# Kernel tuning notes

Measured on AMD Instinct MI355X. Metric: run time of the kernel, lower is better.

Reference implementation:

```python
import jax, jax.numpy as jnp
import numpy as np
import math

PHI = (1.0 + math.sqrt(5.0)) / 2.0
KAPPA = 0.5
B_, L_, D_, N_, R_ = 4, 1024, 768, 16, 48  # batch, seq, d_model, state_size, dt_rank


@jax.custom_vjp
def fractal_pow(mag, exponent):
    # |h|^e with torch _FractalCompress semantics (clamped-ratio grad, no grad wrt e)
    return jnp.maximum(mag, 1e-8) ** exponent


def _fp_fwd(mag, exponent):
    mag_safe = jnp.maximum(mag, 1e-8)
    compressed = mag_safe ** exponent
    ratio = exponent * compressed / (mag_safe + 1e-10)
    return compressed, ratio


def _fp_bwd(ratio, g):
    return (g * jnp.minimum(ratio, 5.0), jnp.zeros_like(ratio))


fractal_pow.defvjp(_fp_fwd, _fp_bwd)


def setup_inputs() -> dict:
    key = jax.random.key(0)
    ks = jax.random.split(key, 7)

    def u(k, shape, fan_in):
        b = (1.0 / PHI) / math.sqrt(fan_in)
        return jax.random.uniform(k, shape, jnp.float32, -b, b)

    x = jax.random.normal(ks[0], (B_, L_, D_), dtype=jnp.float32)
    in_proj_w = u(ks[1], (D_, 2 * D_), D_)          # Linear(D, 2D, bias=False), stored (in,out)
    x_proj_w = u(ks[2], (D_, R_ + 4 * N_), D_)      # Linear(D, dt_rank + 2*N*2, bias=False)
    dt_proj_w = u(ks[3], (R_, D_), R_)              # Linear(dt_rank, D)
    bb = 1.0 / math.sqrt(R_)
    dt_proj_b = jax.random.uniform(ks[4], (D_,), jnp.float32, -bb, bb)
    out_proj_w = u(ks[5], (D_, D_), D_)             # Linear(D, D)
    ob = 1.0 / math.sqrt(D_)
    out_proj_b = jax.random.uniform(ks[6], (D_,), jnp.float32, -ob, ob)
    # phi-scaled A init (exact torch init)
    n_slow = round(N_ / PHI)
    n_fast = N_ - n_slow
    A_init = np.concatenate([np.linspace(0.5, 2.0, n_slow), np.linspace(2.0, float(N_), n_fast)])
    A_log = jnp.asarray(np.log(A_init), dtype=jnp.float32)
    return dict(x=x, in_proj_w=in_proj_w, x_proj_w=x_proj_w, dt_proj_w=dt_proj_w,
                dt_proj_b=dt_proj_b, out_proj_w=out_proj_w, out_proj_b=out_proj_b, A_log=A_log)


def _forward(x, in_proj_w, x_proj_w, dt_proj_w, dt_proj_b, out_proj_w, out_proj_b, A_log):
    B, L, D = x.shape
    N = A_log.shape[0]
    R = dt_proj_w.shape[0]

    xz = x @ in_proj_w                               # (B,L,2D)
    x_in = jax.nn.silu(xz[..., :D])
    z = xz[..., D:]
    xp = x_in @ x_proj_w                             # (B,L,R+4N)
    dt = jax.nn.softplus(xp[..., :R] @ dt_proj_w + dt_proj_b)  # (B,L,D)
    bc = xp[..., R:].reshape(B, L, 2, N, 2)
    Bm, Cm = bc[:, :, 0], bc[:, :, 1]                # (B,L,N,2) each

    # dna_init: 16 phases, magnitude 0.01
    phases = jnp.linspace(0.0, 2.0 * math.pi * (1.0 - 1.0 / N), N)
    h0 = 0.01 * jnp.stack([jnp.cos(phases), jnp.sin(phases)], axis=-1)  # (N,2)
    h0 = jnp.broadcast_to(h0, (B, D, N, 2)) + jnp.zeros((B, D, N, 2), jnp.float32)
    A_neg = -jnp.exp(A_log)                          # (N,)

    def step(h, inp):
        x_t, dt_t, Bt, Ct = inp                      # (B,D),(B,D),(B,N,2),(B,N,2)
        alpha = jnp.exp(dt_t[..., None] * A_neg)     # (B,D,N)
        e = 1.0 + (1.0 - alpha) * KAPPA
        # fractal compress: |h|^e, phase preserved
        mag = jnp.sqrt(h[..., 0] ** 2 + h[..., 1] ** 2 + 1e-8)
        ph = jnp.arctan2(h[..., 1], h[..., 0] + 1e-10)
        cm = fractal_pow(mag, e)
        h = jnp.stack([cm * jnp.cos(ph), cm * jnp.sin(ph)], axis=-1)
        # h += gamma * B * x  (x is real, so complex mul is a scale of B)
        h = h + Bt[:, None, :, :] * (x_t * dt_t)[:, :, None, None]
        # tanh magnitude squash, phase preserved
        m2 = jnp.sqrt(h[..., 0] ** 2 + h[..., 1] ** 2 + 1e-8)
        p2 = jnp.arctan2(h[..., 1], h[..., 0] + 1e-10)
        s = jnp.tanh(m2)
        h = jnp.stack([s * jnp.cos(p2), s * jnp.sin(p2)], axis=-1)
        # y = Re(conj(C) * h).sum(N) = C_re*h_re + C_im*h_im summed over N
        y = jnp.sum(Ct[:, None, :, 0] * h[..., 0] + Ct[:, None, :, 1] * h[..., 1], axis=-1)
        return h, y

    xs = (x_in.swapaxes(0, 1), dt.swapaxes(0, 1), Bm.swapaxes(0, 1), Cm.swapaxes(0, 1))
    _, ys = jax.lax.scan(step, h0, xs)               # ys: (L,B,D)
    y = ys.swapaxes(0, 1) * jax.nn.silu(z)
    return y @ out_proj_w + out_proj_b


def reference(x, in_proj_w, x_proj_w, dt_proj_w, dt_proj_b, out_proj_w, out_proj_b, A_log):
    return _forward(x, in_proj_w, x_proj_w, dt_proj_w, dt_proj_b, out_proj_w, out_proj_b, A_log)
```

## Files before the change

### kernel.cpp

```cpp
#include <hip/hip_runtime.h>
#include <math.h>

#if __has_builtin(__builtin_amdgcn_exp2f)
#define EXP2F(x) __builtin_amdgcn_exp2f(x)
#else
#define EXP2F(x) exp2f(x)
#endif
#if __has_builtin(__builtin_amdgcn_logf)
#define LOG2F(x) __builtin_amdgcn_logf(x)
#else
#define LOG2F(x) log2f(x)
#endif
#if __has_builtin(__builtin_amdgcn_rcpf)
#define RCPF(x) __builtin_amdgcn_rcpf(x)
#else
#define RCPF(x) (1.0f / (x))
#endif

#define LOG2E 1.4426950408889634f

#define DRAIN_VMEM() asm volatile("s_waitcnt vmcnt(0)" ::: "memory")

typedef __bf16 bf16x8 __attribute__((ext_vector_type(8)));
typedef float f32x4 __attribute__((ext_vector_type(4)));

__device__ __forceinline__ float silu_f(float v) {
    return v * RCPF(1.0f + EXP2F(-v * LOG2E));
}
__device__ __forceinline__ float softplus_f(float v) {
    return fmaxf(v, 0.0f) + log1pf(__expf(-fabsf(v)));
}

template <int CTRL>
__device__ __forceinline__ float dpp_add(float v) {
    int r = __builtin_amdgcn_update_dpp(0, __float_as_int(v), CTRL, 0xF, 0xF, true);
    return v + __int_as_float(r);
}

__device__ __forceinline__ unsigned short bf16_rne(float f) {
    unsigned int u = __float_as_uint(f);
    return (unsigned short)((u + 0x7FFFu + ((u >> 16) & 1u)) >> 16);
}
__device__ __forceinline__ unsigned short bf16_hi(float f, float& rem) {
    unsigned int u = __float_as_uint(f);
    unsigned int hb = (u + 0x7FFFu + ((u >> 16) & 1u)) >> 16;
    rem = f - __uint_as_float(hb << 16);
    return (unsigned short)hb;
}

__device__ __forceinline__ void async_g2l16(const void* g, void* l) {
    __builtin_amdgcn_global_load_lds(
        (const __attribute__((address_space(1))) unsigned int*)g,
        (__attribute__((address_space(3))) unsigned int*)l, 16, 0, 0);
}

__global__ __launch_bounds__(256) void conv_all_k(
    const float* __restrict__ x,
    unsigned short* __restrict__ xh,
    const float* __restrict__ w_in,
    unsigned short* __restrict__ wih, unsigned short* __restrict__ wil,
    const float* __restrict__ w_out,
    unsigned short* __restrict__ woh, unsigned short* __restrict__ wol,
    const float* __restrict__ w_xp,
    const float* __restrict__ w_dt,
    const float* __restrict__ b_dt,
    unsigned short* __restrict__ wbh, unsigned short* __restrict__ wbl,
    float* __restrict__ bias_full)
{
    __shared__ float shmem[6272];
    const int bid = blockIdx.x;
    const int t = threadIdx.x;
    if (bid < 768) {
#pragma unroll
        for (int r = 0; r < 4; ++r) {
            int i = (bid + 768 * r) * 256 + t;
            float4 v = ((const float4*)x)[i];
            ushort4 h;
            h.x = bf16_rne(v.x);
            h.y = bf16_rne(v.y);
            h.z = bf16_rne(v.z);
            h.w = bf16_rne(v.w);
            ((ushort4*)xh)[i] = h;
        }
        return;
    }
    if (bid < 2496) {
        const float* W;
        unsigned short *Th, *Tl;
        int N, bx, by;
        if (bid < 1920) {
            int b2 = bid - 768;
            W = w_in; Th = wih; Tl = wil; N = 1536;
            bx = b2 % 48; by = b2 / 48;
        } else {
            int b3 = bid - 1920;
            W = w_out; Th = woh; Tl = wol; N = 768;
            bx = b3 % 24; by = b3 / 24;
        }
        const int K = 768;
        float (*tile)[33] = (float (*)[33])shmem;
        const int tx = t & 31, ty = t >> 5;
        const int n0 = bx * 32, k0 = by * 32;
#pragma unroll
        for (int r = 0; r < 4; ++r)
            tile[ty + r * 8][tx] = W[(size_t)(k0 + ty + r * 8) * N + n0 + tx];
        __syncthreads();
#pragma unroll
        for (int r = 0; r < 4; ++r) {
            float v = tile[tx][ty + r * 8];
            float rem;
            unsigned short h = bf16_hi(v, rem);
            size_t o = (size_t)(n0 + ty + r * 8) * K + k0 + tx;
            Th[o] = h;
            Tl[o] = bf16_rne(rem);
        }
        return;
    }
    if (bid < 2640) {
        int b4 = bid - 2496;
        int bxw = b4 % 12, byw = b4 / 12;
        const int kd0 = byw * 64, dd0 = bxw * 64;
        float* As = shmem;
        float* Ws = shmem + 64 * 49;
        {
            int r = t >> 2;
            int c4 = (t & 3) * 4;
#pragma unroll
            for (int s = 0; s < 3; ++s) {
                float4 a = *(const float4*)&w_xp[(size_t)(kd0 + r) * 112 + c4 + 16 * s];
                As[r * 49 + c4 + 16 * s + 0] = a.x;
                As[r * 49 + c4 + 16 * s + 1] = a.y;
                As[r * 49 + c4 + 16 * s + 2] = a.z;
                As[r * 49 + c4 + 16 * s + 3] = a.w;
            }
            int rw = t >> 4;
            int cw = (t & 15) * 4;
#pragma unroll
            for (int s = 0; s < 3; ++s) {
                float4 w = *(const float4*)&w_dt[(size_t)(rw + 16 * s) * 768 + dd0 + cw];
                Ws[(rw + 16 * s) * 65 + cw + 0] = w.x;
                Ws[(rw + 16 * s) * 65 + cw + 1] = w.y;
                Ws[(rw + 16 * s) * 65 + cw + 2] = w.z;
                Ws[(rw + 16 * s) * 65 + cw + 3] = w.w;
            }
        }
        __syncthreads();
        const int ty = t >> 4, tx = t & 15;
        float acc[4][4];
#pragma unroll
        for (int i = 0; i < 4; ++i)
#pragma unroll
            for (int j = 0; j < 4; ++j) acc[i][j] = 0.0f;
        for (int k = 0; k < 48; ++k) {
            float ar[4], wr[4];
#pragma unroll
            for (int i = 0; i < 4; ++i) ar[i] = As[(ty * 4 + i) * 49 + k];
#pragma unroll
            for (int j = 0; j < 4; ++j) wr[j] = Ws[k * 65 + tx * 4 + j];
#pragma unroll
            for (int i = 0; i < 4; ++i)
#pragma unroll
                for (int j = 0; j < 4; ++j)
                    acc[i][j] = fmaf(ar[i], wr[j], acc[i][j]);
        }
        __syncthreads();
        float* Ot = shmem;
#pragma unroll
        for (int i = 0; i < 4; ++i)
#pragma unroll
            for (int j = 0; j < 4; ++j)
                Ot[(tx * 4 + j) * 65 + ty * 4 + i] = acc[i][j];
        __syncthreads();
        int dl = t >> 2, c0 = (t & 3) * 16;
#pragma unroll
        for (int k = 0; k < 16; ++k) {
            float v = Ot[dl * 65 + c0 + k];
            float rem;
            unsigned short h = bf16_hi(v, rem);
            size_t o = (size_t)(64 + dd0 + dl) * 768 + kd0 + c0 + k;
            wbh[o] = h;
            wbl[o] = bf16_rne(rem);
        }
        return;
    }
    if (bid < 2688) {
        int b5 = bid - 2640;
        int bxb = b5 & 1, byb = b5 >> 1;
        const int n0 = bxb * 32, k0 = byb * 32;
        float (*tile)[33] = (float (*)[33])shmem;
        const int tx = t & 31, ty = t >> 5;
#pragma unroll
        for (int r = 0; r < 4; ++r)
            tile[ty + r * 8][tx] = w_xp[(size_t)(k0 + ty + r * 8) * 112 + 48 + n0 + tx];
        __syncthreads();
#pragma unroll
        for (int r = 0; r < 4; ++r) {
            float v = tile[tx][ty + r * 8];
            float rem;
            unsigned short h = bf16_hi(v, rem);
            size_t o = (size_t)(n0 + ty + r * 8) * 768 + k0 + tx;
            wbh[o] = h;
            wbl[o] = bf16_rne(rem);
        }
        return;
    }
#pragma unroll
    for (int i = 0; i < 4; ++i) {
        int idx = t + 256 * i;
        if (idx < 896)
            bias_full[idx] = (idx >= 64 && idx < 832) ? b_dt[idx - 64] : 0.0f;
    }
}

template <int EPI, int WRX>
__global__ __launch_bounds__(256, 3) void mgemm_k(
    const unsigned short* __restrict__ Ah,
    const unsigned short* __restrict__ Bth, const unsigned short* __restrict__ Btl,
    const float* __restrict__ bias,
    float* __restrict__ C, int K, int ldc, int nby,
    unsigned short* __restrict__ xh, unsigned short* __restrict__ xl)
{
    __shared__ unsigned short smem[2][8192];

    const int t = threadIdx.x;
    const int wave = t >> 6, lane = t & 63;
    const int bx = blockIdx.x / nby, by = blockIdx.x % nby;
    const int bm = by * 128, bn = bx * 64;
    const int mw = (wave >> 1) * 64, nw = (wave & 1) * 32;

    const unsigned short* smat;
    int row0, lmoff;
    if      (wave == 0) { smat = Ah;  row0 = bm;      lmoff = 0; }
    else if (wave == 1) { smat = Ah;  row0 = bm + 64; lmoff = 2048 * 2; }
    else if (wave == 2) { smat = Bth; row0 = bn;      lmoff = 4096 * 2; }
    else                { smat = Btl; row0 = bn;      lmoff = 6144 * 2; }
    const int lr = lane >> 2;
    const int kq = (lane & 3) ^ ((lane >> 3) & 3);
    const unsigned short* gbase = smat + (size_t)(row0 + lr) * K + kq * 8;

    const int la = lane & 15, g4 = lane >> 4;
    const int fo = (g4 ^ ((la >> 1) & 3)) * 8;
    const int aoff = (mw + la) * 32 + fo;
    const int boff = (nw + la) * 32 + fo;

    f32x4 acc[4][2];
#pragma unroll
    for (int i = 0; i < 4; ++i)
#pragma unroll
        for (int j = 0; j < 2; ++j) acc[i][j] = (f32x4){0.f, 0.f, 0.f, 0.f};

    auto stage = [&](int buf, int k0) {
        char* lm = (char*)&smem[buf][0] + lmoff;
        const unsigned short* g = gbase + k0;
#pragma unroll
        for (int j = 0; j < 4; ++j)
            async_g2l16(g + (size_t)j * 16 * K, lm + j * 1024);
    };

    stage(0, 0);
    DRAIN_VMEM();
    __syncthreads();

    for (int k0 = 0; k0 < K; k0 += 32) {
        const int cur = (k0 >> 5) & 1;
        if (k0 + 32 < K) stage(cur ^ 1, k0 + 32);

        const unsigned short* base = &smem[cur][0];
        const unsigned short* pAh = base + aoff;
        const unsigned short* pBh = base + 4096 + boff;
        const unsigned short* pBl = base + 6144 + boff;

        bf16x8 fah[4], fbh[2], fbl[2];
#pragma unroll
        for (int i = 0; i < 4; ++i)
            fah[i] = *(const bf16x8*)(pAh + i * 512);
#pragma unroll
        for (int j = 0; j < 2; ++j) {
            fbh[j] = *(const bf16x8*)(pBh + j * 512);
            fbl[j] = *(const bf16x8*)(pBl + j * 512);
        }
#pragma unroll
        for (int i = 0; i < 4; ++i)
#pragma unroll
            for (int j = 0; j < 2; ++j)
                acc[i][j] = __builtin_amdgcn_mfma_f32_16x16x32_bf16(fah[i], fbh[j], acc[i][j], 0, 0, 0);
#pragma unroll
        for (int i = 0; i < 4; ++i)
#pragma unroll
            for (int j = 0; j < 2; ++j)
                acc[i][j] = __builtin_amdgcn_mfma_f32_16x16x32_bf16(fah[i], fbl[j], acc[i][j], 0, 0, 0);
        DRAIN_VMEM();
        __syncthreads();
    }

#pragma unroll
    for (int i = 0; i < 4; ++i) {
        int row = bm + mw + i * 16 + g4 * 4;
#pragma unroll
        for (int j = 0; j < 2; ++j) {
            int col = bn + nw + j * 16 + la;
            float bz = bias ? bias[col] : 0.0f;
#pragma unroll
            for (int r = 0; r < 4; ++r) {
                float v = acc[i][j][r] + bz;
                if (EPI == 1) v = silu_f(v);
                C[(size_t)(row + r) * ldc + col] = v;
                if (WRX) {
                    if (col < 768) {
                        float rem;
                        unsigned short hh = bf16_hi(v, rem);
                        xh[(size_t)(row + r) * 768 + col] = hh;
                        xl[(size_t)(row + r) * 768 + col] = bf16_rne(rem);
                    }
                }
            }
        }
    }
}

__global__ __launch_bounds__(256, 3) void mgemm3_k(
    const unsigned short* __restrict__ Ahp, const unsigned short* __restrict__ Alp,
    const unsigned short* __restrict__ Bth, const unsigned short* __restrict__ Btl,
    const float* __restrict__ bias,
    float* __restrict__ C, int K, int ldc, int nby)
{
    __shared__ unsigned short smem[2][12288];

    const int t = threadIdx.x;
    const int wave = t >> 6, lane = t & 63;
    const int bx = blockIdx.x / nby, by = blockIdx.x % nby;
    const int bm = by * 128, bn = bx * 64;
    const int mw = (wave >> 1) * 64, nw = (wave & 1) * 32;

    const unsigned short* smat;
    int row0, ninst, lmoff;
    if      (wave == 0) { smat = Ahp; row0 = bm; ninst = 8; lmoff = 0; }
    else if (wave == 1) { smat = Alp; row0 = bm; ninst = 8; lmoff = 8192; }
    else if (wave == 2) { smat = Bth; row0 = bn; ninst = 4; lmoff = 16384; }
    else                { smat = Btl; row0 = bn; ninst = 4; lmoff = 20480; }
    const int lr = lane >> 2;
    const int kq = (lane & 3) ^ ((lane >> 3) & 3);
    const unsigned short* gbase = smat + (size_t)(row0 + lr) * K + kq * 8;

    const int la = lane & 15, g4 = lane >> 4;
    const int fo = (g4 ^ ((la >> 1) & 3)) * 8;
    const int aoff = (mw + la) * 32 + fo;
    const int boff = (nw + la) * 32 + fo;

    f32x4 acc[4][2];
#pragma unroll
    for (int i = 0; i < 4; ++i)
#pragma unroll
        for (int j = 0; j < 2; ++j) acc[i][j] = (f32x4){0.f, 0.f, 0.f, 0.f};

    auto stage = [&](int buf, int k0) {
        char* lm = (char*)&smem[buf][0] + lmoff;
        const unsigned short* g = gbase + k0;
        if (ninst == 8) {
#pragma unroll
            for (int j = 0; j < 8; ++j)
                async_g2l16(g + (size_t)j * 16 * K, lm + j * 1024);
        } else {
#pragma unroll
            for (int j = 0; j < 4; ++j)
                async_g2l16(g + (size_t)j * 16 * K, lm + j * 1024);
        }
    };

    stage(0, 0);
    DRAIN_VMEM();
    __syncthreads();

    for (int k0 = 0; k0 < K; k0 += 32) {
        const int cur = (k0 >> 5) & 1;
        if (k0 + 32 < K) stage(cur ^ 1, k0 + 32);

        const unsigned short* base = &smem[cur][0];
        const unsigned short* pAh = base + aoff;
        const unsigned short* pAl = base + 4096 + aoff;
        const unsigned short* pBh = base + 8192 + boff;
        const unsigned short* pBl = base + 10240 + boff;

        bf16x8 fah[4], fal[4], fbh[2], fbl[2];
#pragma unroll
        for (int i = 0; i < 4; ++i) {
            fah[i] = *(const bf16x8*)(pAh + i * 512);
            fal[i] = *(const bf16x8*)(pAl + i * 512);
        }
#pragma unroll
        for (int j = 0; j < 2; ++j) {
            fbh[j] = *(const bf16x8*)(pBh + j * 512);
            fbl[j] = *(const bf16x8*)(pBl + j * 512);
        }
#pragma unroll
        for (int i = 0; i < 4; ++i)
#pragma unroll
            for (int j = 0; j < 2; ++j)
                acc[i][j] = __builtin_amdgcn_mfma_f32_16x16x32_bf16(fah[i], fbh[j], acc[i][j], 0, 0, 0);
#pragma unroll
        for (int i = 0; i < 4; ++i)
#pragma unroll
            for (int j = 0; j < 2; ++j)
                acc[i][j] = __builtin_amdgcn_mfma_f32_16x16x32_bf16(fah[i], fbl[j], acc[i][j], 0, 0, 0);
#pragma unroll
        for (int i = 0; i < 4; ++i)
#pragma unroll
            for (int j = 0; j < 2; ++j)
                acc[i][j] = __builtin_amdgcn_mfma_f32_16x16x32_bf16(fal[i], fbh[j], acc[i][j], 0, 0, 0);
        DRAIN_VMEM();
        __syncthreads();
    }

#pragma unroll
    for (int i = 0; i < 4; ++i) {
        int row = bm + mw + i * 16 + g4 * 4;
#pragma unroll
        for (int j = 0; j < 2; ++j) {
            int col = bn + nw + j * 16 + la;
            float bz = bias[col];
#pragma unroll
            for (int r = 0; r < 4; ++r) {
                float v = acc[i][j][r] + bz;
                if (col >= 64) v = softplus_f(v);
                C[(size_t)(row + r) * ldc + col] = v;
            }
        }
    }
}

#define L_LEN 1024
#define CH 32
#define NCH (L_LEN / CH)
#define CHP (CH + 4)

__global__ __launch_bounds__(512) void scan_k(
    const float* __restrict__ xz,
    const float* __restrict__ bcdt,
    const float* __restrict__ A_log,
    unsigned short* __restrict__ ybh)
{
    __shared__ float xdt_t[2][16][CHP];
    __shared__ float ds_t[2][16][CHP];
    __shared__ float B0s[2][16][CHP];
    __shared__ float B1s[2][16][CHP];
    __shared__ float C0s[2][16][CHP];
    __shared__ float C1s[2][16][CHP];
    __shared__ float ysp[2][CH][16][8];

    const int t  = threadIdx.x;
    const int b  = blockIdx.y;
    const int d0 = blockIdx.x * 16;
    const size_t rowbase = (size_t)b * L_LEN;
    const bool is_chain = (t < 256);

    const int n  = t & 15;
    const int dl = (t >> 4) & 15;
    const int np = n >> 1;
    float negAl2e = 0.0f, h0 = 0.0f, h1 = 0.0f;
    float s2 = 1.0f, lT = 0.0f;
    if (is_chain) {
        negAl2e = -__expf(A_log[n]) * LOG2E;
        float phase = 6.283185307179586f * (float)n / 16.0f;
        h0 = 0.01f * cosf(phase);
        h1 = 0.01f * sinf(phase);
        lT = LOG2F(fmaf(h0, h0, fmaf(h1, h1, 1e-8f)));
    }

    const int t2 = t - 256;
    const int hl = t2 >> 2;
    const int hf = (t2 & 3) * 4;

    auto stage = [&](int cc) {
        const int bi = cc & 1;
        if (t2 < 128) {
            size_t row = rowbase + cc * CH + hl;
            float4 rx = *(const float4*)&xz[row * 1536 + d0 + hf];
            float4 rd = *(const float4*)&bcdt[row * 896 + 64 + d0 + hf];
            xdt_t[bi][hf + 0][hl] = rx.x * rd.x;
            xdt_t[bi][hf + 1][hl] = rx.y * rd.y;
            xdt_t[bi][hf + 2][hl] = rx.z * rd.z;
            xdt_t[bi][hf + 3][hl] = rx.w * rd.w;
            ds_t[bi][hf + 0][hl] = rd.x;
            ds_t[bi][hf + 1][hl] = rd.y;
            ds_t[bi][hf + 2][hl] = rd.z;
            ds_t[bi][hf + 3][hl] = rd.w;
        }
#pragma unroll
        for (int i = 0; i < 2; ++i) {
            int idx = t2 + 256 * i;
            int lb = idx >> 4, j4 = (idx & 15) * 4;
            float4 rbc = *(const float4*)&bcdt[(rowbase + cc * CH + lb) * 896 + j4];
            if (j4 < 32) {
                int nn = j4 >> 1;
                B0s[bi][nn][lb]     = rbc.x;
                B1s[bi][nn][lb]     = rbc.y;
                B0s[bi][nn + 1][lb] = rbc.z;
                B1s[bi][nn + 1][lb] = rbc.w;
            } else {
                int nn = (j4 - 32) >> 1;
                C0s[bi][nn][lb]     = rbc.x;
                C1s[bi][nn][lb]     = rbc.y;
                C0s[bi][nn + 1][lb] = rbc.z;
                C1s[bi][nn + 1][lb] = rbc.w;
            }
        }
    };

    auto store_y = [&](int cs) {
        if (t2 >= 128) return;
        const int bi = cs & 1;
        size_t row = rowbase + cs * CH + hl;
        float4 zq = *(const float4*)&xz[row * 1536 + 768 + d0 + hf];
        float yr[4];
#pragma unroll
        for (int j = 0; j < 4; ++j) {
            float4 p0 = *(const float4*)&ysp[bi][hl][hf + j][0];
            float4 p1 = *(const float4*)&ysp[bi][hl][hf + j][4];
            yr[j] = ((p0.x + p0.y) + (p0.z + p0.w)) + ((p1.x + p1.y) + (p1.z + p1.w));
        }
        ushort4 hh;
        hh.x = bf16_rne(yr[0] * zq.x);
        hh.y = bf16_rne(yr[1] * zq.y);
        hh.z = bf16_rne(yr[2] * zq.z);
        hh.w = bf16_rne(yr[3] * zq.w);
        *(ushort4*)&ybh[row * 768 + d0 + hf] = hh;
    };

    if (!is_chain) stage(0);
    __syncthreads();

    for (int c = 0; c < NCH; ++c) {
        if (is_chain) {
            __builtin_amdgcn_s_setprio(1);
            const int bi = c & 1;
            const float* xr  = &xdt_t[bi][dl][0];
            const float* dr  = &ds_t[bi][dl][0];
            const float* b0r = &B0s[bi][n][0];
            const float* b1r = &B1s[bi][n][0];
            const float* c0r = &C0s[bi][n][0];
            const float* c1r = &C1s[bi][n][0];

            float4 px  = *(const float4*)(xr);
            float4 pd  = *(const float4*)(dr);
            float4 pb0 = *(const float4*)(b0r);
            float4 pb1 = *(const float4*)(b1r);
            float4 pc0 = *(const float4*)(c0r);
            float4 pc1 = *(const float4*)(c1r);

            for (int l4 = 0; l4 < CH; l4 += 4) {
                float4 cx = px, cd = pd, cb0 = pb0, cb1 = pb1, cc0 = pc0, cc1 = pc1;
                if (l4 + 4 < CH) {
                    px  = *(const float4*)(xr  + l4 + 4);
                    pd  = *(const float4*)(dr  + l4 + 4);
                    pb0 = *(const float4*)(b0r + l4 + 4);
                    pb1 = *(const float4*)(b1r + l4 + 4);
                    pc0 = *(const float4*)(c0r + l4 + 4);
                    pc1 = *(const float4*)(c1r + l4 + 4);
                }
                const float xv[4]  = {cx.x,  cx.y,  cx.z,  cx.w};
                const float dv[4]  = {cd.x,  cd.y,  cd.z,  cd.w};
                const float C0v[4] = {cc0.x, cc0.y, cc0.z, cc0.w};
                const float C1v[4] = {cc1.x, cc1.y, cc1.z, cc1.w};

                float cfv[4], bx0[4], bx1[4];
                const float B0v[4] = {cb0.x, cb0.y, cb0.z, cb0.w};
                const float B1v[4] = {cb1.x, cb1.y, cb1.z, cb1.w};
#pragma unroll
                for (int u = 0; u < 4; ++u) {
                    cfv[u] = fmaf(EXP2F(dv[u] * negAl2e), -0.25f, 0.25f);
                    bx0[u] = B0v[u] * xv[u];
                    bx1[u] = B1v[u] * xv[u];
                }

#pragma unroll
                for (int u = 0; u < 4; ++u) {
                    float g = s2 * EXP2F(cfv[u] * lT);
                    h0 = fmaf(h0, g, bx0[u]);
                    h1 = fmaf(h1, g, bx1[u]);
                    float q  = fmaf(h0, h0, fmaf(h1, h1, 1e-8f));
                    float q2 = q * q;
                    float num = fmaf(q2, q + 378.0f,              fmaf(17325.0f, q, 135135.0f));
                    float den = fmaf(q2, fmaf(28.0f, q, 3150.0f), fmaf(62370.0f, q, 135135.0f));
                    s2 = num * RCPF(den);
                    lT = LOG2F(s2 * s2 * q);

                    float yv = s2 * fmaf(C0v[u], h0, C1v[u] * h1);
                    yv = dpp_add<0xB1>(yv);
                    if ((n & 1) == 0) ysp[bi][l4 + u][dl][np] = yv;
                }
            }
            __builtin_amdgcn_s_setprio(0);
        } else {
            if (c + 1 < NCH) stage(c + 1);
            if (c >= 1) store_y(c - 1);
        }
        __syncthreads();
    }
    if (!is_chain) store_y(NCH - 1);
}

extern "C" void kernel_launch(void* const* d_in, const int* in_sizes, int n_in,
                              void* d_out, int out_size, void* d_ws, size_t ws_size,
                              hipStream_t stream)
{
    const float* x     = (const float*)d_in[0];
    const float* w_in  = (const float*)d_in[1];
    const float* w_xp  = (const float*)d_in[2];
    const float* w_dt  = (const float*)d_in[3];
    const float* b_dt  = (const float*)d_in[4];
    const float* w_out = (const float*)d_in[5];
    const float* b_out = (const float*)d_in[6];
    const float* A_log = (const float*)d_in[7];
    float* out = (float*)d_out;

    const int M = 4096;
    float* xz        = (float*)d_ws;
    float* bcdt      = xz + (size_t)M * 1536;
    float* bias_full = bcdt + (size_t)M * 896;
    unsigned short* ah   = (unsigned short*)(bias_full + 896);
    unsigned short* ybh  = ah   + (size_t)M * 768;
    unsigned short* xinh = ybh  + (size_t)M * 768;
    unsigned short* xinl = xinh + (size_t)M * 768;
    unsigned short* wh   = xinl + (size_t)M * 768;
    unsigned short* wl   = wh   + (size_t)1536 * 768;
    unsigned short* voh  = wl   + (size_t)1536 * 768;
    unsigned short* vol  = voh  + (size_t)768 * 768;
    unsigned short* wbh  = vol  + (size_t)768 * 768;
    unsigned short* wbl  = wbh  + (size_t)896 * 768;

    dim3 blk(256);

    conv_all_k<<<dim3(2689), blk, 0, stream>>>(
        x, ah, w_in, wh, wl, w_out, voh, vol,
        w_xp, w_dt, b_dt, wbh, wbl, bias_full);

    mgemm_k<1, 1><<<dim3(24 * 32), blk, 0, stream>>>(
        ah, wh, wl, (const float*)nullptr, xz, 768, 1536, 32, xinh, xinl);

    mgemm3_k<<<dim3(14 * 32), blk, 0, stream>>>(
        xinh, xinl, wbh, wbl, bias_full, bcdt, 768, 896, 32);

    scan_k<<<dim3(48, 4), dim3(512), 0, stream>>>(xz, bcdt, A_log, ybh);

    mgemm_k<0, 0><<<dim3(12 * 32), blk, 0, stream>>>(
        ybh, voh, vol, b_out, out, 768, 768, 32,
        (unsigned short*)nullptr, (unsigned short*)nullptr);
}
```

Baseline: 255.9 us.

## Triple-buffer LDS staging in split-bf16 GEMMs with partial vmcnt waits

Both MFMA GEMM kernels go from double to triple buffering of shared memory. Loads are issued two k-steps ahead, and each iteration waits only for the older batch of async loads (vmcnt(4) or vmcnt(8)) instead of draining every load. One barrier per iteration now sits before staging, which replaces the end-of-loop drain. This hides more global-load latency behind the MFMA work, at the cost of more LDS per block, and the launch-bounds occupancy hint for mgemm3_k drops from 3 to 2.

```diff
diff --git a/kernel.cpp b/kernel.cpp
--- a/kernel.cpp
+++ b/kernel.cpp
@@ -19,7 +19,9 @@
 
 #define LOG2E 1.4426950408889634f
 
-#define DRAIN_VMEM() asm volatile("s_waitcnt vmcnt(0)" ::: "memory")
+#define WAITVM0() asm volatile("s_waitcnt vmcnt(0)" ::: "memory")
+#define WAITVM4() asm volatile("s_waitcnt vmcnt(4)" ::: "memory")
+#define WAITVM8() asm volatile("s_waitcnt vmcnt(8)" ::: "memory")
 
 typedef __bf16 bf16x8 __attribute__((ext_vector_type(8)));
 typedef float f32x4 __attribute__((ext_vector_type(4)));
@@ -220,7 +222,7 @@
     float* __restrict__ C, int K, int ldc, int nby,
     unsigned short* __restrict__ xh, unsigned short* __restrict__ xl)
 {
-    __shared__ unsigned short smem[2][8192];
+    __shared__ unsigned short smem[3][8192];
 
     const int t = threadIdx.x;
     const int wave = t >> 6, lane = t & 63;
@@ -231,9 +233,9 @@
     const unsigned short* smat;
     int row0, lmoff;
     if      (wave == 0) { smat = Ah;  row0 = bm;      lmoff = 0; }
-    else if (wave == 1) { smat = Ah;  row0 = bm + 64; lmoff = 2048 * 2; }
-    else if (wave == 2) { smat = Bth; row0 = bn;      lmoff = 4096 * 2; }
-    else                { smat = Btl; row0 = bn;      lmoff = 6144 * 2; }
+    else if (wave == 1) { smat = Ah;  row0 = bm + 64; lmoff = 4096; }
+    else if (wave == 2) { smat = Bth; row0 = bn;      lmoff = 8192; }
+    else                { smat = Btl; row0 = bn;      lmoff = 12288; }
     const int lr = lane >> 2;
     const int kq = (lane & 3) ^ ((lane >> 3) & 3);
     const unsigned short* gbase = smat + (size_t)(row0 + lr) * K + kq * 8;
@@ -258,12 +260,16 @@
     };
 
     stage(0, 0);
-    DRAIN_VMEM();
-    __syncthreads();
-
+    if (32 < K) stage(1, 32);
+
+    int cur = 0, stg = 2;
     for (int k0 = 0; k0 < K; k0 += 32) {
-        const int cur = (k0 >> 5) & 1;
-        if (k0 + 32 < K) stage(cur ^ 1, k0 + 32);
+        if (k0 + 32 < K) { WAITVM4(); } else { WAITVM0(); }
+        __syncthreads();
+        if (k0 + 64 < K) {
+            stage(stg, k0 + 64);
+            stg = (stg == 2) ? 0 : stg + 1;
+        }
 
         const unsigned short* base = &smem[cur][0];
         const unsigned short* pAh = base + aoff;
@@ -289,8 +295,7 @@
 #pragma unroll
             for (int j = 0; j < 2; ++j)
                 acc[i][j] = __builtin_amdgcn_mfma_f32_16x16x32_bf16(fah[i], fbl[j], acc[i][j], 0, 0, 0);
-        DRAIN_VMEM();
-        __syncthreads();
+        cur = (cur == 2) ? 0 : cur + 1;
     }
 
 #pragma unroll
@@ -318,13 +323,13 @@
     }
 }
 
-__global__ __launch_bounds__(256, 3) void mgemm3_k(
+__global__ __launch_bounds__(256, 2) void mgemm3_k(
     const unsigned short* __restrict__ Ahp, const unsigned short* __restrict__ Alp,
     const unsigned short* __restrict__ Bth, const unsigned short* __restrict__ Btl,
     const float* __restrict__ bias,
     float* __restrict__ C, int K, int ldc, int nby)
 {
-    __shared__ unsigned short smem[2][12288];
+    __shared__ unsigned short smem[3][12288];
 
     const int t = threadIdx.x;
     const int wave = t >> 6, lane = t & 63;
@@ -368,12 +373,20 @@
     };
 
     stage(0, 0);
-    DRAIN_VMEM();
-    __syncthreads();
-
+    if (32 < K) stage(1, 32);
+
+    int cur = 0, stg = 2;
     for (int k0 = 0; k0 < K; k0 += 32) {
-        const int cur = (k0 >> 5) & 1;
-        if (k0 + 32 < K) stage(cur ^ 1, k0 + 32);
+        if (k0 + 32 < K) {
+            if (ninst == 8) { WAITVM8(); } else { WAITVM4(); }
+        } else {
+            WAITVM0();
+        }
+        __syncthreads();
+        if (k0 + 64 < K) {
+            stage(stg, k0 + 64);
+            stg = (stg == 2) ? 0 : stg + 1;
+        }
 
         const unsigned short* base = &smem[cur][0];
         const unsigned short* pAh = base + aoff;
@@ -407,8 +420,7 @@
 #pragma unroll
             for (int j = 0; j < 2; ++j)
                 acc[i][j] = __builtin_amdgcn_mfma_f32_16x16x32_bf16(fal[i], fbh[j], acc[i][j], 0, 0, 0);
-        DRAIN_VMEM();
-        __syncthreads();
+        cur = (cur == 2) ? 0 : cur + 1;
     }
 
 #pragma unroll
```

New measurement: 257.2 us. No clear change (+0.5%).

## Split weight conversion, fuse side conversions into in-proj GEMM, narrow GEMM tiles

Applied to the files above, without the earlier changes.

The combined conversion kernel is split. Only the x and in_proj conversions stay in front; the out_proj, x_proj/dt_proj and bias preparation move into extra blocks appended to the in_proj GEMM launch, so they run alongside it. The x_proj GEMM and the out_proj GEMM drop to 32-wide N tiles, which doubles their block counts so more CUs are busy. The trade-off is less reuse of each A tile per block and a less uniform mixed-work launch.

```diff
diff --git a/kernel.cpp b/kernel.cpp
--- a/kernel.cpp
+++ b/kernel.cpp
@@ -54,20 +54,13 @@
         (__attribute__((address_space(3))) unsigned int*)l, 16, 0, 0);
 }
 
-__global__ __launch_bounds__(256) void conv_all_k(
+__global__ __launch_bounds__(256) void conv_front_k(
     const float* __restrict__ x,
     unsigned short* __restrict__ xh,
     const float* __restrict__ w_in,
-    unsigned short* __restrict__ wih, unsigned short* __restrict__ wil,
-    const float* __restrict__ w_out,
-    unsigned short* __restrict__ woh, unsigned short* __restrict__ wol,
-    const float* __restrict__ w_xp,
-    const float* __restrict__ w_dt,
-    const float* __restrict__ b_dt,
-    unsigned short* __restrict__ wbh, unsigned short* __restrict__ wbl,
-    float* __restrict__ bias_full)
+    unsigned short* __restrict__ wih, unsigned short* __restrict__ wil)
 {
-    __shared__ float shmem[6272];
+    __shared__ float shmem[32 * 33];
     const int bid = blockIdx.x;
     const int t = threadIdx.x;
     if (bid < 768) {
@@ -84,40 +77,164 @@
         }
         return;
     }
-    if (bid < 2496) {
-        const float* W;
-        unsigned short *Th, *Tl;
-        int N, bx, by;
-        if (bid < 1920) {
-            int b2 = bid - 768;
-            W = w_in; Th = wih; Tl = wil; N = 1536;
-            bx = b2 % 48; by = b2 / 48;
-        } else {
-            int b3 = bid - 1920;
-            W = w_out; Th = woh; Tl = wol; N = 768;
-            bx = b3 % 24; by = b3 / 24;
-        }
-        const int K = 768;
+    int b2 = bid - 768;
+    const int N = 1536, K = 768;
+    float (*tile)[33] = (float (*)[33])shmem;
+    const int tx = t & 31, ty = t >> 5;
+    const int bx = b2 % 48, by = b2 / 48;
+    const int n0 = bx * 32, k0 = by * 32;
+#pragma unroll
+    for (int r = 0; r < 4; ++r)
+        tile[ty + r * 8][tx] = w_in[(size_t)(k0 + ty + r * 8) * N + n0 + tx];
+    __syncthreads();
+#pragma unroll
+    for (int r = 0; r < 4; ++r) {
+        float v = tile[tx][ty + r * 8];
+        float rem;
+        unsigned short h = bf16_hi(v, rem);
+        size_t o = (size_t)(n0 + ty + r * 8) * K + k0 + tx;
+        wih[o] = h;
+        wil[o] = bf16_rne(rem);
+    }
+}
+
+__global__ __launch_bounds__(256, 3) void gemm2t_k(
+    const unsigned short* __restrict__ Ah,
+    const unsigned short* __restrict__ Bth, const unsigned short* __restrict__ Btl,
+    float* __restrict__ C,
+    unsigned short* __restrict__ xh, unsigned short* __restrict__ xl,
+    const float* __restrict__ w_out,
+    unsigned short* __restrict__ woh, unsigned short* __restrict__ wol,
+    const float* __restrict__ w_xp,
+    const float* __restrict__ w_dt,
+    const float* __restrict__ b_dt,
+    unsigned short* __restrict__ wbh, unsigned short* __restrict__ wbl,
+    float* __restrict__ bias_full)
+{
+    __shared__ unsigned short smem[2][8192];
+
+    const int t = threadIdx.x;
+    const int bid = blockIdx.x;
+    const int K = 768, ldc = 1536, nby = 32;
+
+    if (bid < 768) {
+        const int wave = t >> 6, lane = t & 63;
+        const int bx = bid / nby, by = bid % nby;
+        const int bm = by * 128, bn = bx * 64;
+        const int mw = (wave >> 1) * 64, nw = (wave & 1) * 32;
+
+        const unsigned short* smat;
+        int row0, lmoff;
+        if      (wave == 0) { smat = Ah;  row0 = bm;      lmoff = 0; }
+        else if (wave == 1) { smat = Ah;  row0 = bm + 64; lmoff = 4096; }
+        else if (wave == 2) { smat = Bth; row0 = bn;      lmoff = 8192; }
+        else                { smat = Btl; row0 = bn;      lmoff = 12288; }
+        const int lr = lane >> 2;
+        const int kq = (lane & 3) ^ ((lane >> 3) & 3);
+        const unsigned short* gbase = smat + (size_t)(row0 + lr) * K + kq * 8;
+
+        const int la = lane & 15, g4 = lane >> 4;
+        const int fo = (g4 ^ ((la >> 1) & 3)) * 8;
+        const int aoff = (mw + la) * 32 + fo;
+        const int boff = (nw + la) * 32 + fo;
+
+        f32x4 acc[4][2];
+#pragma unroll
+        for (int i = 0; i < 4; ++i)
+#pragma unroll
+            for (int j = 0; j < 2; ++j) acc[i][j] = (f32x4){0.f, 0.f, 0.f, 0.f};
+
+        auto stage = [&](int buf, int k0) {
+            char* lm = (char*)&smem[buf][0] + lmoff;
+            const unsigned short* g = gbase + k0;
+#pragma unroll
+            for (int j = 0; j < 4; ++j)
+                async_g2l16(g + (size_t)j * 16 * K, lm + j * 1024);
+        };
+
+        stage(0, 0);
+        DRAIN_VMEM();
+        __syncthreads();
+
+        for (int k0 = 0; k0 < K; k0 += 32) {
+            const int cur = (k0 >> 5) & 1;
+            if (k0 + 32 < K) stage(cur ^ 1, k0 + 32);
+
+            const unsigned short* base = &smem[cur][0];
+            const unsigned short* pAh = base + aoff;
+            const unsigned short* pBh = base + 4096 + boff;
+            const unsigned short* pBl = base + 6144 + boff;
+
+            bf16x8 fah[4], fbh[2], fbl[2];
+#pragma unroll
+            for (int i = 0; i < 4; ++i)
+                fah[i] = *(const bf16x8*)(pAh + i * 512);
+#pragma unroll
+            for (int j = 0; j < 2; ++j) {
+                fbh[j] = *(const bf16x8*)(pBh + j * 512);
+                fbl[j] = *(const bf16x8*)(pBl + j * 512);
+            }
+#pragma unroll
+            for (int i = 0; i < 4; ++i)
+#pragma unroll
+                for (int j = 0; j < 2; ++j)
+                    acc[i][j] = __builtin_amdgcn_mfma_f32_16x16x32_bf16(fah[i], fbh[j], acc[i][j], 0, 0, 0);
+#pragma unroll
+            for (int i = 0; i < 4; ++i)
+#pragma unroll
+                for (int j = 0; j < 2; ++j)
+                    acc[i][j] = __builtin_amdgcn_mfma_f32_16x16x32_bf16(fah[i], fbl[j], acc[i][j], 0, 0, 0);
+            DRAIN_VMEM();
+            __syncthreads();
+        }
+
+#pragma unroll
+        for (int i = 0; i < 4; ++i) {
+            int row = bm + mw + i * 16 + g4 * 4;
+#pragma unroll
+            for (int j = 0; j < 2; ++j) {
+                int col = bn + nw + j * 16 + la;
+#pragma unroll
+                for (int r = 0; r < 4; ++r) {
+                    float v = silu_f(acc[i][j][r]);
+                    C[(size_t)(row + r) * ldc + col] = v;
+                    if (col < 768) {
+                        float rem;
+                        unsigned short hh = bf16_hi(v, rem);
+                        xh[(size_t)(row + r) * 768 + col] = hh;
+                        xl[(size_t)(row + r) * 768 + col] = bf16_rne(rem);
+                    }
+                }
+            }
+        }
+        return;
+    }
+
+    float* shmem = (float*)&smem[0][0];
+    const int tb = bid - 768;
+    if (tb < 576) {
+        const int N = 768, K2 = 768;
         float (*tile)[33] = (float (*)[33])shmem;
         const int tx = t & 31, ty = t >> 5;
+        const int bx = tb % 24, by = tb / 24;
         const int n0 = bx * 32, k0 = by * 32;
 #pragma unroll
         for (int r = 0; r < 4; ++r)
-            tile[ty + r * 8][tx] = W[(size_t)(k0 + ty + r * 8) * N + n0 + tx];
+            tile[ty + r * 8][tx] = w_out[(size_t)(k0 + ty + r * 8) * N + n0 + tx];
         __syncthreads();
 #pragma unroll
         for (int r = 0; r < 4; ++r) {
             float v = tile[tx][ty + r * 8];
             float rem;
             unsigned short h = bf16_hi(v, rem);
-            size_t o = (size_t)(n0 + ty + r * 8) * K + k0 + tx;
-            Th[o] = h;
-            Tl[o] = bf16_rne(rem);
+            size_t o = (size_t)(n0 + ty + r * 8) * K2 + k0 + tx;
+            woh[o] = h;
+            wol[o] = bf16_rne(rem);
         }
         return;
     }
-    if (bid < 2640) {
-        int b4 = bid - 2496;
+    if (tb < 720) {
+        int b4 = tb - 576;
         int bxw = b4 % 12, byw = b4 / 12;
         const int kd0 = byw * 64, dd0 = bxw * 64;
         float* As = shmem;
@@ -183,8 +300,8 @@
         }
         return;
     }
-    if (bid < 2688) {
-        int b5 = bid - 2640;
+    if (tb < 768) {
+        int b5 = tb - 720;
         int bxb = b5 & 1, byb = b5 >> 1;
         const int n0 = bxb * 32, k0 = byb * 32;
         float (*tile)[33] = (float (*)[33])shmem;
@@ -212,132 +329,26 @@
     }
 }
 
-template <int EPI, int WRX>
-__global__ __launch_bounds__(256, 3) void mgemm_k(
-    const unsigned short* __restrict__ Ah,
-    const unsigned short* __restrict__ Bth, const unsigned short* __restrict__ Btl,
-    const float* __restrict__ bias,
-    float* __restrict__ C, int K, int ldc, int nby,
-    unsigned short* __restrict__ xh, unsigned short* __restrict__ xl)
-{
-    __shared__ unsigned short smem[2][8192];
-
-    const int t = threadIdx.x;
-    const int wave = t >> 6, lane = t & 63;
-    const int bx = blockIdx.x / nby, by = blockIdx.x % nby;
-    const int bm = by * 128, bn = bx * 64;
-    const int mw = (wave >> 1) * 64, nw = (wave & 1) * 32;
-
-    const unsigned short* smat;
-    int row0, lmoff;
-    if      (wave == 0) { smat = Ah;  row0 = bm;      lmoff = 0; }
-    else if (wave == 1) { smat = Ah;  row0 = bm + 64; lmoff = 2048 * 2; }
-    else if (wave == 2) { smat = Bth; row0 = bn;      lmoff = 4096 * 2; }
-    else                { smat = Btl; row0 = bn;      lmoff = 6144 * 2; }
-    const int lr = lane >> 2;
-    const int kq = (lane & 3) ^ ((lane >> 3) & 3);
-    const unsigned short* gbase = smat + (size_t)(row0 + lr) * K + kq * 8;
-
-    const int la = lane & 15, g4 = lane >> 4;
-    const int fo = (g4 ^ ((la >> 1) & 3)) * 8;
-    const int aoff = (mw + la) * 32 + fo;
-    const int boff = (nw + la) * 32 + fo;
-
-    f32x4 acc[4][2];
-#pragma unroll
-    for (int i = 0; i < 4; ++i)
-#pragma unroll
-        for (int j = 0; j < 2; ++j) acc[i][j] = (f32x4){0.f, 0.f, 0.f, 0.f};
-
-    auto stage = [&](int buf, int k0) {
-        char* lm = (char*)&smem[buf][0] + lmoff;
-        const unsigned short* g = gbase + k0;
-#pragma unroll
-        for (int j = 0; j < 4; ++j)
-            async_g2l16(g + (size_t)j * 16 * K, lm + j * 1024);
-    };
-
-    stage(0, 0);
-    DRAIN_VMEM();
-    __syncthreads();
-
-    for (int k0 = 0; k0 < K; k0 += 32) {
-        const int cur = (k0 >> 5) & 1;
-        if (k0 + 32 < K) stage(cur ^ 1, k0 + 32);
-
-        const unsigned short* base = &smem[cur][0];
-        const unsigned short* pAh = base + aoff;
-        const unsigned short* pBh = base + 4096 + boff;
-        const unsigned short* pBl = base + 6144 + boff;
-
-        bf16x8 fah[4], fbh[2], fbl[2];
-#pragma unroll
-        for (int i = 0; i < 4; ++i)
-            fah[i] = *(const bf16x8*)(pAh + i * 512);
-#pragma unroll
-        for (int j = 0; j < 2; ++j) {
-            fbh[j] = *(const bf16x8*)(pBh + j * 512);
-            fbl[j] = *(const bf16x8*)(pBl + j * 512);
-        }
-#pragma unroll
-        for (int i = 0; i < 4; ++i)
-#pragma unroll
-            for (int j = 0; j < 2; ++j)
-                acc[i][j] = __builtin_amdgcn_mfma_f32_16x16x32_bf16(fah[i], fbh[j], acc[i][j], 0, 0, 0);
-#pragma unroll
-        for (int i = 0; i < 4; ++i)
-#pragma unroll
-            for (int j = 0; j < 2; ++j)
-                acc[i][j] = __builtin_amdgcn_mfma_f32_16x16x32_bf16(fah[i], fbl[j], acc[i][j], 0, 0, 0);
-        DRAIN_VMEM();
-        __syncthreads();
-    }
-
-#pragma unroll
-    for (int i = 0; i < 4; ++i) {
-        int row = bm + mw + i * 16 + g4 * 4;
-#pragma unroll
-        for (int j = 0; j < 2; ++j) {
-            int col = bn + nw + j * 16 + la;
-            float bz = bias ? bias[col] : 0.0f;
-#pragma unroll
-            for (int r = 0; r < 4; ++r) {
-                float v = acc[i][j][r] + bz;
-                if (EPI == 1) v = silu_f(v);
-                C[(size_t)(row + r) * ldc + col] = v;
-                if (WRX) {
-                    if (col < 768) {
-                        float rem;
-                        unsigned short hh = bf16_hi(v, rem);
-                        xh[(size_t)(row + r) * 768 + col] = hh;
-                        xl[(size_t)(row + r) * 768 + col] = bf16_rne(rem);
-                    }
-                }
-            }
-        }
-    }
-}
-
 __global__ __launch_bounds__(256, 3) void mgemm3_k(
     const unsigned short* __restrict__ Ahp, const unsigned short* __restrict__ Alp,
     const unsigned short* __restrict__ Bth, const unsigned short* __restrict__ Btl,
     const float* __restrict__ bias,
     float* __restrict__ C, int K, int ldc, int nby)
 {
-    __shared__ unsigned short smem[2][12288];
+    __shared__ unsigned short smem[2][10240];
 
     const int t = threadIdx.x;
     const int wave = t >> 6, lane = t & 63;
     const int bx = blockIdx.x / nby, by = blockIdx.x % nby;
-    const int bm = by * 128, bn = bx * 64;
-    const int mw = (wave >> 1) * 64, nw = (wave & 1) * 32;
+    const int bm = by * 128, bn = bx * 32;
+    const int mw = (wave >> 1) * 64, nw = (wave & 1) * 16;
 
     const unsigned short* smat;
     int row0, ninst, lmoff;
     if      (wave == 0) { smat = Ahp; row0 = bm; ninst = 8; lmoff = 0; }
     else if (wave == 1) { smat = Alp; row0 = bm; ninst = 8; lmoff = 8192; }
-    else if (wave == 2) { smat = Bth; row0 = bn; ninst = 4; lmoff = 16384; }
-    else                { smat = Btl; row0 = bn; ninst = 4; lmoff = 20480; }
+    else if (wave == 2) { smat = Bth; row0 = bn; ninst = 2; lmoff = 16384; }
+    else                { smat = Btl; row0 = bn; ninst = 2; lmoff = 18432; }
     const int lr = lane >> 2;
     const int kq = (lane & 3) ^ ((lane >> 3) & 3);
     const unsigned short* gbase = smat + (size_t)(row0 + lr) * K + kq * 8;
@@ -347,11 +358,9 @@
     const int aoff = (mw + la) * 32 + fo;
     const int boff = (nw + la) * 32 + fo;
 
-    f32x4 acc[4][2];
-#pragma unroll
-    for (int i = 0; i < 4; ++i)
-#pragma unroll
-        for (int j = 0; j < 2; ++j) acc[i][j] = (f32x4){0.f, 0.f, 0.f, 0.f};
+    f32x4 acc[4];
+#pragma unroll
+    for (int i = 0; i < 4; ++i) acc[i] = (f32x4){0.f, 0.f, 0.f, 0.f};
 
     auto stage = [&](int buf, int k0) {
         char* lm = (char*)&smem[buf][0] + lmoff;
@@ -362,7 +371,7 @@
                 async_g2l16(g + (size_t)j * 16 * K, lm + j * 1024);
         } else {
 #pragma unroll
-            for (int j = 0; j < 4; ++j)
+            for (int j = 0; j < 2; ++j)
                 async_g2l16(g + (size_t)j * 16 * K, lm + j * 1024);
         }
     };
@@ -379,34 +388,25 @@
         const unsigned short* pAh = base + aoff;
         const unsigned short* pAl = base + 4096 + aoff;
         const unsigned short* pBh = base + 8192 + boff;
-        const unsigned short* pBl = base + 10240 + boff;
-
-        bf16x8 fah[4], fal[4], fbh[2], fbl[2];
+        const unsigned short* pBl = base + 9216 + boff;
+
+        bf16x8 fah[4], fal[4], fbh, fbl;
 #pragma unroll
         for (int i = 0; i < 4; ++i) {
             fah[i] = *(const bf16x8*)(pAh + i * 512);
             fal[i] = *(const bf16x8*)(pAl + i * 512);
         }
-#pragma unroll
-        for (int j = 0; j < 2; ++j) {
-            fbh[j] = *(const bf16x8*)(pBh + j * 512);
-            fbl[j] = *(const bf16x8*)(pBl + j * 512);
-        }
-#pragma unroll
-        for (int i = 0; i < 4; ++i)
-#pragma unroll
-            for (int j = 0; j < 2; ++j)
-                acc[i][j] = __builtin_amdgcn_mfma_f32_16x16x32_bf16(fah[i], fbh[j], acc[i][j], 0, 0, 0);
-#pragma unroll
-        for (int i = 0; i < 4; ++i)
-#pragma unroll
-            for (int j = 0; j < 2; ++j)
-                acc[i][j] = __builtin_amdgcn_mfma_f32_16x16x32_bf16(fah[i], fbl[j], acc[i][j], 0, 0, 0);
-#pragma unroll
-        for (int i = 0; i < 4; ++i)
-#pragma unroll
-            for (int j = 0; j < 2; ++j)
-                acc[i][j] = __builtin_amdgcn_mfma_f32_16x16x32_bf16(fal[i], fbh[j], acc[i][j], 0, 0, 0);
+        fbh = *(const bf16x8*)(pBh);
+        fbl = *(const bf16x8*)(pBl);
+#pragma unroll
+        for (int i = 0; i < 4; ++i)
+            acc[i] = __builtin_amdgcn_mfma_f32_16x16x32_bf16(fah[i], fbh, acc[i], 0, 0, 0);
+#pragma unroll
+        for (int i = 0; i < 4; ++i)
+            acc[i] = __builtin_amdgcn_mfma_f32_16x16x32_bf16(fah[i], fbl, acc[i], 0, 0, 0);
+#pragma unroll
+        for (int i = 0; i < 4; ++i)
+            acc[i] = __builtin_amdgcn_mfma_f32_16x16x32_bf16(fal[i], fbh, acc[i], 0, 0, 0);
         DRAIN_VMEM();
         __syncthreads();
     }
@@ -414,17 +414,101 @@
 #pragma unroll
     for (int i = 0; i < 4; ++i) {
         int row = bm + mw + i * 16 + g4 * 4;
-#pragma unroll
-        for (int j = 0; j < 2; ++j) {
-            int col = bn + nw + j * 16 + la;
-            float bz = bias[col];
-#pragma unroll
-            for (int r = 0; r < 4; ++r) {
-                float v = acc[i][j][r] + bz;
-                if (col >= 64) v = softplus_f(v);
-                C[(size_t)(row + r) * ldc + col] = v;
-            }
-        }
+        int col = bn + nw + la;
+        float bz = bias[col];
+#pragma unroll
+        for (int r = 0; r < 4; ++r) {
+            float v = acc[i][r] + bz;
+            if (col >= 64) v = softplus_f(v);
+            C[(size_t)(row + r) * ldc + col] = v;
+        }
+    }
+}
+
+__global__ __launch_bounds__(256, 3) void mgemm_out_k(
+    const unsigned short* __restrict__ Ah,
+    const unsigned short* __restrict__ Bth, const unsigned short* __restrict__ Btl,
+    const float* __restrict__ bias,
+    float* __restrict__ C, int K, int ldc, int nby)
+{
+    __shared__ unsigned short smem[2][6144];
+
+    const int t = threadIdx.x;
+    const int wave = t >> 6, lane = t & 63;
+    const int bx = blockIdx.x / nby, by = blockIdx.x % nby;
+    const int bm = by * 128, bn = bx * 32;
+    const int mw = (wave >> 1) * 64, nw = (wave & 1) * 16;
+
+    const unsigned short* smat;
+    int row0, ninst, lmoff;
+    if      (wave == 0) { smat = Ah;  row0 = bm;      ninst = 4; lmoff = 0; }
+    else if (wave == 1) { smat = Ah;  row0 = bm + 64; ninst = 4; lmoff = 4096; }
+    else if (wave == 2) { smat = Bth; row0 = bn;      ninst = 2; lmoff = 8192; }
+    else                { smat = Btl; row0 = bn;      ninst = 2; lmoff = 10240; }
+    const int lr = lane >> 2;
+    const int kq = (lane & 3) ^ ((lane >> 3) & 3);
+    const unsigned short* gbase = smat + (size_t)(row0 + lr) * K + kq * 8;
+
+    const int la = lane & 15, g4 = lane >> 4;
+    const int fo = (g4 ^ ((la >> 1) & 3)) * 8;
+    const int aoff = (mw + la) * 32 + fo;
+    const int boff = (nw + la) * 32 + fo;
+
+    f32x4 acc[4];
+#pragma unroll
+    for (int i = 0; i < 4; ++i) acc[i] = (f32x4){0.f, 0.f, 0.f, 0.f};
+
+    auto stage = [&](int buf, int k0) {
+        char* lm = (char*)&smem[buf][0] + lmoff;
+        const unsigned short* g = gbase + k0;
+        if (ninst == 4) {
+#pragma unroll
+            for (int j = 0; j < 4; ++j)
+                async_g2l16(g + (size_t)j * 16 * K, lm + j * 1024);
+        } else {
+#pragma unroll
+            for (int j = 0; j < 2; ++j)
+                async_g2l16(g + (size_t)j * 16 * K, lm + j * 1024);
+        }
+    };
+
+    stage(0, 0);
+    DRAIN_VMEM();
+    __syncthreads();
+
+    for (int k0 = 0; k0 < K; k0 += 32) {
+        const int cur = (k0 >> 5) & 1;
+        if (k0 + 32 < K) stage(cur ^ 1, k0 + 32);
+
+        const unsigned short* base = &smem[cur][0];
+        const unsigned short* pAh = base + aoff;
+        const unsigned short* pBh = base + 4096 + boff;
+        const unsigned short* pBl = base + 5120 + boff;
+
+        bf16x8 fah[4], fbh, fbl;
+#pragma unroll
+        for (int i = 0; i < 4; ++i)
+            fah[i] = *(const bf16x8*)(pAh + i * 512);
+        fbh = *(const bf16x8*)(pBh);
+        fbl = *(const bf16x8*)(pBl);
+#pragma unroll
+        for (int i = 0; i < 4; ++i)
+            acc[i] = __builtin_amdgcn_mfma_f32_16x16x32_bf16(fah[i], fbh, acc[i], 0, 0, 0);
+#pragma unroll
+        for (int i = 0; i < 4; ++i)
+            acc[i] = __builtin_amdgcn_mfma_f32_16x16x32_bf16(fah[i], fbl, acc[i], 0, 0, 0);
+        DRAIN_VMEM();
+        __syncthreads();
+    }
+
+#pragma unroll
+    for (int i = 0; i < 4; ++i) {
+        int row = bm + mw + i * 16 + g4 * 4;
+        int col = bn + nw + la;
+        float bz = bias[col];
+#pragma unroll
+        for (int r = 0; r < 4; ++r)
+            C[(size_t)(row + r) * ldc + col] = acc[i][r] + bz;
     }
 }
 
@@ -630,19 +714,17 @@
 
     dim3 blk(256);
 
-    conv_all_k<<<dim3(2689), blk, 0, stream>>>(
-        x, ah, w_in, wh, wl, w_out, voh, vol,
-        w_xp, w_dt, b_dt, wbh, wbl, bias_full);
-
-    mgemm_k<1, 1><<<dim3(24 * 32), blk, 0, stream>>>(
-        ah, wh, wl, (const float*)nullptr, xz, 768, 1536, 32, xinh, xinl);
-
-    mgemm3_k<<<dim3(14 * 32), blk, 0, stream>>>(
+    conv_front_k<<<dim3(1920), blk, 0, stream>>>(x, ah, w_in, wh, wl);
+
+    gemm2t_k<<<dim3(1537), blk, 0, stream>>>(
+        ah, wh, wl, xz, xinh, xinl,
+        w_out, voh, vol, w_xp, w_dt, b_dt, wbh, wbl, bias_full);
+
+    mgemm3_k<<<dim3(28 * 32), blk, 0, stream>>>(
         xinh, xinl, wbh, wbl, bias_full, bcdt, 768, 896, 32);
 
     scan_k<<<dim3(48, 4), dim3(512), 0, stream>>>(xz, bcdt, A_log, ybh);
 
-    mgemm_k<0, 0><<<dim3(12 * 32), blk, 0, stream>>>(
-        ybh, voh, vol, b_out, out, 768, 768, 32,
-        (unsigned short*)nullptr, (unsigned short*)nullptr);
-}
+    mgemm_out_k<<<dim3(24 * 32), blk, 0, stream>>>(
+        ybh, voh, vol, b_out, out, 768, 768, 32);
+}
```

After: 256.6 us. Within noise of the previous version (+0.3%).
